# Optimization experiments

Hardware: AMD Instinct MI355X
Metric: run time of the kernel (lower is better)

## Reference

```python
import jax, jax.numpy as jnp
import numpy as np

H = 256  # LSTM hidden units per layer

def _cell(xt, h, c, W, U, b):
    # Keras LSTMCell: gate order i, f, g(cell), o; sigmoid recurrent activation, tanh activation
    z = xt @ W + h @ U + b  # (B, 4H)
    i, f, g, o = jnp.split(z, 4, axis=-1)
    c_new = jax.nn.sigmoid(f) * c + jax.nn.sigmoid(i) * jnp.tanh(g)
    h_new = jax.nn.sigmoid(o) * jnp.tanh(c_new)
    return h_new, c_new

def _stacked_lstm(x, W1, U1, b1, W2, U2, b2):
    # x: (B, T, F). Returns concat of FINAL CELL STATES of both layers: (B, 2H)
    # (original code takes outputs[i+1][1], i.e. the c state of each LSTMCell)
    B = x.shape[0]
    def step(carry, xt):
        h1, c1, h2, c2 = carry
        h1, c1 = _cell(xt, h1, c1, W1, U1, b1)
        h2, c2 = _cell(h1, h2, c2, W2, U2, b2)
        return (h1, c1, h2, c2), None
    z0 = jnp.zeros((B, H), x.dtype)
    (h1, c1, h2, c2), _ = jax.lax.scan(step, (z0, z0, z0, z0), jnp.swapaxes(x, 0, 1))
    return jnp.concatenate([c1, c2], axis=-1)

def _glorot(key, shape):
    lim = np.sqrt(6.0 / (shape[0] + shape[1]))
    return jax.random.uniform(key, shape, jnp.float32, -lim, lim)

def _lstm_bias():
    # Keras unit_forget_bias=True: forget-gate bias initialized to 1
    return jnp.zeros((4 * H,), jnp.float32).at[H:2 * H].set(1.0)

def setup_inputs():
    key = jax.random.key(0)
    ks = jax.random.split(key, 16)
    B, T, F, ZD = 16384, 20, 80, 32
    inp = {
        "x": jax.random.normal(ks[0], (B, T, F), jnp.float32),
        "eps1": jax.random.normal(ks[1], (B, ZD), jnp.float32),
        "eps2": jax.random.normal(ks[2], (B, ZD), jnp.float32),
        # z2 stacked LSTM (input F)
        "z2_W1": _glorot(ks[3], (F, 4 * H)), "z2_U1": _glorot(ks[4], (H, 4 * H)), "z2_b1": _lstm_bias(),
        "z2_W2": _glorot(ks[5], (H, 4 * H)), "z2_U2": _glorot(ks[6], (H, 4 * H)), "z2_b2": _lstm_bias(),
        # z1 stacked LSTM (input F + z2_dim)
        "z1_W1": _glorot(ks[7], (F + ZD, 4 * H)), "z1_U1": _glorot(ks[8], (H, 4 * H)), "z1_b1": _lstm_bias(),
        "z1_W2": _glorot(ks[9], (H, 4 * H)), "z1_U2": _glorot(ks[10], (H, 4 * H)), "z1_b2": _lstm_bias(),
        # dense heads (input 2H -> ZD), linear (mu_nl=logvar_nl=None)
        "mu2_W": _glorot(ks[11], (2 * H, ZD)), "mu2_b": jnp.zeros((ZD,), jnp.float32),
        "lv2_W": _glorot(ks[12], (2 * H, ZD)), "lv2_b": jnp.zeros((ZD,), jnp.float32),
        "mu1_W": _glorot(ks[13], (2 * H, ZD)), "mu1_b": jnp.zeros((ZD,), jnp.float32),
        "lv1_W": _glorot(ks[14], (2 * H, ZD)), "lv1_b": jnp.zeros((ZD,), jnp.float32),
    }
    return inp

def reference(x, eps1, eps2,
              z2_W1, z2_U1, z2_b1, z2_W2, z2_U2, z2_b2,
              z1_W1, z1_U1, z1_b1, z1_W2, z1_U2, z1_b2,
              mu2_W, mu2_b, lv2_W, lv2_b, mu1_W, mu1_b, lv1_W, lv1_b):
    B, T, _ = x.shape
    # z2 branch
    z2_pre = _stacked_lstm(x, z2_W1, z2_U1, z2_b1, z2_W2, z2_U2, z2_b2)  # (B, 2H)
    z2_mu = z2_pre @ mu2_W + mu2_b
    z2_logvar = z2_pre @ lv2_W + lv2_b
    z2_sample = eps2 * jnp.exp(0.5 * z2_logvar) + z2_mu  # reparameterize
    # z1 branch: tile z2_sample over time, concat with x
    z2_tiled = jnp.broadcast_to(z2_sample[:, None, :], (B, T, z2_sample.shape[-1]))
    x_z2 = jnp.concatenate([x, z2_tiled], axis=-1)  # (B, T, F+ZD)
    z1_pre = _stacked_lstm(x_z2, z1_W1, z1_U1, z1_b1, z1_W2, z1_U2, z1_b2)
    z1_mu = z1_pre @ mu1_W + mu1_b
    z1_logvar = z1_pre @ lv1_W + lv1_b
    z1_sample = eps1 * jnp.exp(0.5 * z1_logvar) + z1_mu
    return (z1_mu, z1_logvar, z1_sample, z2_mu, z2_logvar, z2_sample)
```

## Files before the change

kernel.cpp:

```cpp
#include <hip/hip_runtime.h>
#include <hip/hip_bf16.h>

#define B_SZ 16384
#define T_SZ 20

typedef __attribute__((ext_vector_type(8))) __bf16 bf16x8;
typedef __attribute__((ext_vector_type(4))) float f32x4;

__device__ __forceinline__ float sigm(float x){ return 1.f/(1.f+__expf(-x)); }
__device__ __forceinline__ float tanh_(float x){ return 1.f-2.f/(__expf(2.f*x)+1.f); }

#define OFF_L1Z2 0
#define OFF_L2Z2 360448
#define OFF_L1Z1 884736
#define OFF_L2Z1 1277952
#define OFF_HZ2  1802240
#define OFF_HZ1  1835008
#define WP_TOT   1867776

__global__ void prep_w(const float* __restrict__ W0, const float* __restrict__ U0,
                       const float* __restrict__ W1, const float* __restrict__ U1,
                       const float* __restrict__ W2, const float* __restrict__ U2,
                       const float* __restrict__ W3, const float* __restrict__ U3,
                       const float* __restrict__ muW2, const float* __restrict__ lvW2,
                       const float* __restrict__ muW1, const float* __restrict__ lvW1,
                       __bf16* __restrict__ wp)
{
    int idx = blockIdx.x * 256 + threadIdx.x;
    if (idx >= WP_TOT) return;
    if (idx < OFF_HZ2) {
        const float *W, *U;
        int Fx, Kx, KT, local;
        if (idx < OFF_L2Z2)      { W = W0; U = U0; Fx = 80;  Kx = 96;  KT = 11; local = idx; }
        else if (idx < OFF_L1Z1) { W = W1; U = U1; Fx = 256; Kx = 256; KT = 16; local = idx - OFF_L2Z2; }
        else if (idx < OFF_L2Z1) { W = W2; U = U2; Fx = 112; Kx = 128; KT = 12; local = idx - OFF_L1Z1; }
        else                     { W = W3; U = U3; Fx = 256; Kx = 256; KT = 16; local = idx - OFF_L2Z1; }
        int jj = local & 7, lane = (local >> 3) & 63, nt8 = (local >> 9) & 7, rest = local >> 12;
        int kt = rest % KT, wgn = rest / KT;
        int gate = nt8 >> 1, hh = nt8 & 1;
        int n = gate * 256 + wgn * 32 + hh * 16 + (lane & 15);
        int k = kt * 32 + ((lane >> 4) << 3) + jj;
        float v = (k < Fx) ? W[k * 1024 + n] : (k < Kx ? 0.f : U[(k - Kx) * 1024 + n]);
        wp[idx] = (__bf16)v;
    } else {
        int base = (idx < OFF_HZ1) ? OFF_HZ2 : OFF_HZ1;
        const float* mw = (idx < OFF_HZ1) ? muW2 : muW1;
        const float* lw = (idx < OFF_HZ1) ? lvW2 : lvW1;
        int local = idx - base;
        int jj = local & 7, lane = (local >> 3) & 63, nt = (local >> 9) & 3, kt = local >> 11;
        int k = kt * 32 + ((lane >> 4) << 3) + jj;
        int c16 = lane & 15;
        float v = (nt < 2) ? mw[k * 32 + nt * 16 + c16] : lw[k * 32 + (nt - 2) * 16 + c16];
        wp[idx] = (__bf16)v;
    }
}

__global__ void xconv(const float* __restrict__ x, __bf16* __restrict__ xb)
{
    int idx = blockIdx.x * 256 + threadIdx.x;
    int c8 = idx & 15, row = idx >> 4;
    bf16x8 r;
    if (c8 < 10) {
        const float4* p = reinterpret_cast<const float4*>(x + (size_t)row * 80 + c8 * 8);
        float4 u0 = p[0], u1 = p[1];
        r[0]=(__bf16)u0.x; r[1]=(__bf16)u0.y; r[2]=(__bf16)u0.z; r[3]=(__bf16)u0.w;
        r[4]=(__bf16)u1.x; r[5]=(__bf16)u1.y; r[6]=(__bf16)u1.z; r[7]=(__bf16)u1.w;
    } else {
#pragma unroll
        for (int i = 0; i < 8; ++i) r[i] = (__bf16)0.f;
    }
    *reinterpret_cast<bf16x8*>(xb + (size_t)row * 128 + c8 * 8) = r;
}

__global__ void bcast_z2(const __bf16* __restrict__ z2sb, __bf16* __restrict__ xb)
{
    int idx = blockIdx.x * 256 + threadIdx.x;
    int g = idx & 3, b = idx >> 2;
    bf16x8 v = *reinterpret_cast<const bf16x8*>(z2sb + (size_t)b * 32 + g * 8);
#pragma unroll
    for (int t = 0; t < T_SZ; ++t)
        *reinterpret_cast<bf16x8*>(xb + ((size_t)b * T_SZ + t) * 128 + 80 + g * 8) = v;
}

__device__ __forceinline__ void stage16(const __bf16* g, __bf16* l)
{
    __builtin_amdgcn_global_load_lds(
        (const __attribute__((address_space(1))) unsigned*)g,
        (__attribute__((address_space(3))) unsigned*)l, 16, 0, 0);
}

template <int KT, int KTP, int XKT, int TWOH, int FIRST>
__global__ void __launch_bounds__(256, 4)
step_gemm(const __bf16* __restrict__ xb, int t,
          const __bf16* __restrict__ hA, const __bf16* __restrict__ hB,
          const __bf16* __restrict__ wpm, const float* __restrict__ bias,
          float* __restrict__ cbuf, __bf16* __restrict__ hout)
{
    constexpr int P = (KT + 1) / 2;
    __shared__ __align__(16) __bf16 Bs[4][4096];

    const int tid = threadIdx.x;
    const int w = tid >> 6, lane = tid & 63;
    const int r16 = lane & 15, kq = lane >> 4;
    const int mid = blockIdx.x & 127, wgn = blockIdx.x >> 7;
    const int rb = mid * 128 + w * 32;
    const __bf16* wpB = wpm + (size_t)wgn * KTP * 4096;

    const __bf16 *x0 = nullptr, *x1 = nullptr;
    if (XKT > 0) {
        x0 = xb + ((size_t)(rb + r16) * T_SZ + t) * 128;
        x1 = xb + ((size_t)(rb + 16 + r16) * T_SZ + t) * 128;
    }
    const __bf16* hA0 = hA + (size_t)(rb + r16) * 256;
    const __bf16* hA1 = hA + (size_t)(rb + 16 + r16) * 256;
    const __bf16* hB0 = TWOH ? hB + (size_t)(rb + r16) * 256 : nullptr;
    const __bf16* hB1 = TWOH ? hB + (size_t)(rb + 16 + r16) * 256 : nullptr;

    f32x4 acc[8][2];
#pragma unroll
    for (int nt = 0; nt < 8; ++nt)
#pragma unroll
        for (int m = 0; m < 2; ++m) acc[nt][m] = f32x4{0.f, 0.f, 0.f, 0.f};

    auto aptr = [&](int kt, int m) -> const __bf16* {
        if (kt < XKT) return (m ? x1 : x0) + kt * 32 + kq * 8;
        int kk = kt - XKT;
        if (!TWOH || kk < 8) return (m ? hA1 : hA0) + kk * 32 + kq * 8;
        return (m ? hB1 : hB0) + (kk - 8) * 32 + kq * 8;
    };
    auto loadPh = [&](int k0, bf16x8* a) {
        a[0] = *reinterpret_cast<const bf16x8*>(aptr(k0, 0));
        a[1] = *reinterpret_cast<const bf16x8*>(aptr(k0, 1));
        if (k0 + 1 < KT) {
            a[2] = *reinterpret_cast<const bf16x8*>(aptr(k0 + 1, 0));
            a[3] = *reinterpret_cast<const bf16x8*>(aptr(k0 + 1, 1));
        }
    };
    auto compPh = [&](int k0, const bf16x8* a) {
        {
            const __bf16* bp = &Bs[k0 & 3][lane * 8];
#pragma unroll
            for (int nt = 0; nt < 8; ++nt) {
                bf16x8 bv = *reinterpret_cast<const bf16x8*>(bp + nt * 512);
                acc[nt][0] = __builtin_amdgcn_mfma_f32_16x16x32_bf16(a[0], bv, acc[nt][0], 0, 0, 0);
                acc[nt][1] = __builtin_amdgcn_mfma_f32_16x16x32_bf16(a[1], bv, acc[nt][1], 0, 0, 0);
            }
        }
        if (k0 + 1 < KT) {
            const __bf16* bp = &Bs[(k0 + 1) & 3][lane * 8];
#pragma unroll
            for (int nt = 0; nt < 8; ++nt) {
                bf16x8 bv = *reinterpret_cast<const bf16x8*>(bp + nt * 512);
                acc[nt][0] = __builtin_amdgcn_mfma_f32_16x16x32_bf16(a[2], bv, acc[nt][0], 0, 0, 0);
                acc[nt][1] = __builtin_amdgcn_mfma_f32_16x16x32_bf16(a[3], bv, acc[nt][1], 0, 0, 0);
            }
        }
    };
    auto stageKt = [&](int kt) {
        const __bf16* g = wpB + (size_t)kt * 4096 + tid * 8;
        stage16(g, &Bs[kt & 3][tid * 8]);
        stage16(g + 2048, &Bs[kt & 3][2048 + tid * 8]);
    };

    bf16x8 aP[2][4];
    stageKt(0);
    if (KT > 1) stageKt(1);
    loadPh(0, aP[0]);
    __syncthreads();

#pragma unroll
    for (int p = 0; p < P; ++p) {
        const int ks = 2 * p + 2;
        if (ks < KT)     stageKt(ks);
        if (ks + 1 < KT) stageKt(ks + 1);
        if (ks < KT)     loadPh(ks, aP[(p + 1) & 1]);
        compPh(2 * p, aP[p & 1]);
        __syncthreads();
    }

    float bg[2][4];
#pragma unroll
    for (int hh = 0; hh < 2; ++hh)
#pragma unroll
        for (int gate = 0; gate < 4; ++gate)
            bg[hh][gate] = bias[gate * 256 + wgn * 32 + hh * 16 + r16];

#pragma unroll
    for (int m = 0; m < 2; ++m)
#pragma unroll
        for (int hh = 0; hh < 2; ++hh) {
            const int hcol = wgn * 32 + hh * 16 + r16;
            f32x4 zi = acc[0 + hh][m], zf = acc[2 + hh][m], zg = acc[4 + hh][m], zo = acc[6 + hh][m];
#pragma unroll
            for (int q = 0; q < 4; ++q) {
                int row = rb + m * 16 + kq * 4 + q;
                size_t off = (size_t)row * 256 + hcol;
                float cn;
                if (FIRST) {
                    cn = sigm(zi[q] + bg[hh][0]) * tanh_(zg[q] + bg[hh][2]);
                } else {
                    float co = cbuf[off];
                    cn = sigm(zf[q] + bg[hh][1]) * co
                       + sigm(zi[q] + bg[hh][0]) * tanh_(zg[q] + bg[hh][2]);
                }
                cbuf[off] = cn;
                hout[off] = (__bf16)(sigm(zo[q] + bg[hh][3]) * tanh_(cn));
            }
        }
}

__global__ void __launch_bounds__(128, 4)
head_mfma(const float* __restrict__ c1, const float* __restrict__ c2,
          const __bf16* __restrict__ hp, const float* __restrict__ mub,
          const float* __restrict__ lvb, const float* __restrict__ eps,
          float* __restrict__ omu, float* __restrict__ olv, float* __restrict__ osm,
          __bf16* __restrict__ osb)
{
    const int tid = threadIdx.x;
    const int w = tid >> 6, lane = tid & 63;
    const int r16 = lane & 15, kq = lane >> 4;
    const int rb = blockIdx.x * 64 + w * 32;

    f32x4 acc[4][2];
#pragma unroll
    for (int nt = 0; nt < 4; ++nt)
#pragma unroll
        for (int m = 0; m < 2; ++m) acc[nt][m] = f32x4{0.f, 0.f, 0.f, 0.f};

#pragma unroll
    for (int kt = 0; kt < 16; ++kt) {
        const float* cs = (kt < 8) ? c1 : c2;
        int k = (kt & 7) * 32 + kq * 8;
        bf16x8 a[2];
#pragma unroll
        for (int m = 0; m < 2; ++m) {
            const float* pr = cs + (size_t)(rb + m * 16 + r16) * 256 + k;
            float4 u0 = reinterpret_cast<const float4*>(pr)[0];
            float4 u1 = reinterpret_cast<const float4*>(pr)[1];
            a[m][0]=(__bf16)u0.x; a[m][1]=(__bf16)u0.y; a[m][2]=(__bf16)u0.z; a[m][3]=(__bf16)u0.w;
            a[m][4]=(__bf16)u1.x; a[m][5]=(__bf16)u1.y; a[m][6]=(__bf16)u1.z; a[m][7]=(__bf16)u1.w;
        }
        const __bf16* hb = hp + kt * 2048 + lane * 8;
#pragma unroll
        for (int nt = 0; nt < 4; ++nt) {
            bf16x8 bv = *reinterpret_cast<const bf16x8*>(hb + nt * 512);
            acc[nt][0] = __builtin_amdgcn_mfma_f32_16x16x32_bf16(a[0], bv, acc[nt][0], 0, 0, 0);
            acc[nt][1] = __builtin_amdgcn_mfma_f32_16x16x32_bf16(a[1], bv, acc[nt][1], 0, 0, 0);
        }
    }

#pragma unroll
    for (int m = 0; m < 2; ++m)
#pragma unroll
        for (int q = 0; q < 4; ++q) {
            int row = rb + m * 16 + kq * 4 + q;
#pragma unroll
            for (int z = 0; z < 2; ++z) {
                int zc = z * 16 + r16;
                float mu = acc[z][m][q] + mub[zc];
                float lv = acc[z + 2][m][q] + lvb[zc];
                int idx = row * 32 + zc;
                omu[idx] = mu;
                olv[idx] = lv;
                float s = fmaf(eps[idx], expf(0.5f * lv), mu);
                osm[idx] = s;
                if (osb) osb[idx] = (__bf16)s;
            }
        }
}

extern "C" void kernel_launch(void* const* d_in, const int* in_sizes, int n_in,
                              void* d_out, int out_size, void* d_ws, size_t ws_size,
                              hipStream_t stream)
{
    const float* x    = (const float*)d_in[0];
    const float* eps1 = (const float*)d_in[1];
    const float* eps2 = (const float*)d_in[2];
    const float* z2W1 = (const float*)d_in[3];
    const float* z2U1 = (const float*)d_in[4];
    const float* z2b1 = (const float*)d_in[5];
    const float* z2W2 = (const float*)d_in[6];
    const float* z2U2 = (const float*)d_in[7];
    const float* z2b2 = (const float*)d_in[8];
    const float* z1W1 = (const float*)d_in[9];
    const float* z1U1 = (const float*)d_in[10];
    const float* z1b1 = (const float*)d_in[11];
    const float* z1W2 = (const float*)d_in[12];
    const float* z1U2 = (const float*)d_in[13];
    const float* z1b2 = (const float*)d_in[14];
    const float* mu2W = (const float*)d_in[15];
    const float* mu2b = (const float*)d_in[16];
    const float* lv2W = (const float*)d_in[17];
    const float* lv2b = (const float*)d_in[18];
    const float* mu1W = (const float*)d_in[19];
    const float* mu1b = (const float*)d_in[20];
    const float* lv1W = (const float*)d_in[21];
    const float* lv1b = (const float*)d_in[22];

    char* ws = (char*)d_ws;
    __bf16* wp   = (__bf16*)ws;
    __bf16* z2sb = (__bf16*)(ws + 4194304);
    __bf16* xb   = (__bf16*)(ws + 5242880);
    __bf16* h1a  = (__bf16*)(ws + 89128960);
    __bf16* h2a  = (__bf16*)(ws + 97517568);
    __bf16* h1b  = (__bf16*)(ws + 105906176);
    __bf16* h2b  = (__bf16*)(ws + 114294784);
    float*  c1   = (float*)(ws + 122683392);
    float*  c2   = (float*)(ws + 139460608);

    __bf16* h1[2] = {h1a, h1b};
    __bf16* h2[2] = {h2a, h2b};

    float* out = (float*)d_out;
    const int BZ = B_SZ * 32;
    float* z1mu = out;           float* z1lv = out + BZ;     float* z1sm = out + 2 * BZ;
    float* z2mu = out + 3 * BZ;  float* z2lv = out + 4 * BZ; float* z2sm = out + 5 * BZ;

    xconv<<<B_SZ * T_SZ * 16 / 256, 256, 0, stream>>>(x, xb);
    prep_w<<<7296, 256, 0, stream>>>(z2W1, z2U1, z2W2, z2U2, z1W1, z1U1, z1W2, z1U2,
                                     mu2W, lv2W, mu1W, lv1W, wp);

    step_gemm<3, 11, 3, 0, 1><<<1024, 256, 0, stream>>>(xb, 0, h1a, nullptr,
                                                        wp + OFF_L1Z2, z2b1, c1, h1[0]);
    step_gemm<8, 16, 0, 1, 1><<<1024, 256, 0, stream>>>(xb, 0, h1[0], h2a,
                                                        wp + OFF_L2Z2, z2b2, c2, h2[0]);
    for (int t = 1; t < T_SZ; ++t) {
        int cur = t & 1, prv = cur ^ 1;
        step_gemm<11, 11, 3, 0, 0><<<1024, 256, 0, stream>>>(xb, t, h1[prv], nullptr,
                                                             wp + OFF_L1Z2, z2b1, c1, h1[cur]);
        step_gemm<16, 16, 0, 1, 0><<<1024, 256, 0, stream>>>(xb, t, h1[cur], h2[prv],
                                                             wp + OFF_L2Z2, z2b2, c2, h2[cur]);
    }
    head_mfma<<<256, 128, 0, stream>>>(c1, c2, wp + OFF_HZ2, mu2b, lv2b, eps2,
                                       z2mu, z2lv, z2sm, z2sb);
    bcast_z2<<<B_SZ * 4 / 256, 256, 0, stream>>>(z2sb, xb);

    step_gemm<4, 12, 4, 0, 1><<<1024, 256, 0, stream>>>(xb, 0, h1a, nullptr,
                                                        wp + OFF_L1Z1, z1b1, c1, h1[0]);
    step_gemm<8, 16, 0, 1, 1><<<1024, 256, 0, stream>>>(xb, 0, h1[0], h2a,
                                                        wp + OFF_L2Z1, z1b2, c2, h2[0]);
    for (int t = 1; t < T_SZ; ++t) {
        int cur = t & 1, prv = cur ^ 1;
        step_gemm<12, 12, 4, 0, 0><<<1024, 256, 0, stream>>>(xb, t, h1[prv], nullptr,
                                                             wp + OFF_L1Z1, z1b1, c1, h1[cur]);
        step_gemm<16, 16, 0, 1, 0><<<1024, 256, 0, stream>>>(xb, t, h1[cur], h2[prv],
                                                             wp + OFF_L2Z1, z1b2, c2, h2[cur]);
    }
    head_mfma<<<256, 128, 0, stream>>>(c1, c2, wp + OFF_HZ1, mu1b, lv1b, eps1,
                                       z1mu, z1lv, z1sm, nullptr);
}
```

Before: 2.373 ms.

## Restructure step GEMM k-loop into per-tile pipeline with fine-grained vmcnt waits

Replaces the two-k-tile phase loop with a per-k-tile software pipeline that prefetches weights and A fragments two tiles ahead. It uses explicit s_waitcnt vmcnt counts plus a raw s_barrier and sched_barriers instead of __syncthreads, so outstanding loads for later tiles are not drained each step. It also folds the kq offset into the base pointers. The LDS ring has 4 slots with a distance-2 prefetch, which looks safe, but the hand-computed vmcnt values assume a fixed ordering of load instructions. If the compiler emits loads in a different order, correctness or overlap could suffer.

```diff
diff --git a/kernel.cpp b/kernel.cpp
--- a/kernel.cpp
+++ b/kernel.cpp
@@ -96,7 +96,6 @@
           const __bf16* __restrict__ wpm, const float* __restrict__ bias,
           float* __restrict__ cbuf, __bf16* __restrict__ hout)
 {
-    constexpr int P = (KT + 1) / 2;
     __shared__ __align__(16) __bf16 Bs[4][4096];
 
     const int tid = threadIdx.x;
@@ -108,13 +107,16 @@
 
     const __bf16 *x0 = nullptr, *x1 = nullptr;
     if (XKT > 0) {
-        x0 = xb + ((size_t)(rb + r16) * T_SZ + t) * 128;
-        x1 = xb + ((size_t)(rb + 16 + r16) * T_SZ + t) * 128;
-    }
-    const __bf16* hA0 = hA + (size_t)(rb + r16) * 256;
-    const __bf16* hA1 = hA + (size_t)(rb + 16 + r16) * 256;
-    const __bf16* hB0 = TWOH ? hB + (size_t)(rb + r16) * 256 : nullptr;
-    const __bf16* hB1 = TWOH ? hB + (size_t)(rb + 16 + r16) * 256 : nullptr;
+        x0 = xb + ((size_t)(rb + r16) * T_SZ + t) * 128 + kq * 8;
+        x1 = xb + ((size_t)(rb + 16 + r16) * T_SZ + t) * 128 + kq * 8;
+    }
+    const __bf16* hA0 = hA + (size_t)(rb + r16) * 256 + kq * 8;
+    const __bf16* hA1 = hA + (size_t)(rb + 16 + r16) * 256 + kq * 8;
+    const __bf16 *hB0 = nullptr, *hB1 = nullptr;
+    if (TWOH) {
+        hB0 = hB + (size_t)(rb + r16) * 256 + kq * 8;
+        hB1 = hB + (size_t)(rb + 16 + r16) * 256 + kq * 8;
+    }
 
     f32x4 acc[8][2];
 #pragma unroll
@@ -122,61 +124,44 @@
 #pragma unroll
         for (int m = 0; m < 2; ++m) acc[nt][m] = f32x4{0.f, 0.f, 0.f, 0.f};
 
-    auto aptr = [&](int kt, int m) -> const __bf16* {
-        if (kt < XKT) return (m ? x1 : x0) + kt * 32 + kq * 8;
+    bf16x8 aR[3][2];
+
+    auto ap = [&](int kt, int m) -> const __bf16* {
+        if (XKT > 0 && kt < XKT) return (m ? x1 : x0) + kt * 32;
         int kk = kt - XKT;
-        if (!TWOH || kk < 8) return (m ? hA1 : hA0) + kk * 32 + kq * 8;
-        return (m ? hB1 : hB0) + (kk - 8) * 32 + kq * 8;
+        if (!TWOH || kk < 8) return (m ? hA1 : hA0) + kk * 32;
+        return (m ? hB1 : hB0) + (kk - 8) * 32;
     };
-    auto loadPh = [&](int k0, bf16x8* a) {
-        a[0] = *reinterpret_cast<const bf16x8*>(aptr(k0, 0));
-        a[1] = *reinterpret_cast<const bf16x8*>(aptr(k0, 1));
-        if (k0 + 1 < KT) {
-            a[2] = *reinterpret_cast<const bf16x8*>(aptr(k0 + 1, 0));
-            a[3] = *reinterpret_cast<const bf16x8*>(aptr(k0 + 1, 1));
-        }
-    };
-    auto compPh = [&](int k0, const bf16x8* a) {
-        {
-            const __bf16* bp = &Bs[k0 & 3][lane * 8];
-#pragma unroll
-            for (int nt = 0; nt < 8; ++nt) {
-                bf16x8 bv = *reinterpret_cast<const bf16x8*>(bp + nt * 512);
-                acc[nt][0] = __builtin_amdgcn_mfma_f32_16x16x32_bf16(a[0], bv, acc[nt][0], 0, 0, 0);
-                acc[nt][1] = __builtin_amdgcn_mfma_f32_16x16x32_bf16(a[1], bv, acc[nt][1], 0, 0, 0);
-            }
-        }
-        if (k0 + 1 < KT) {
-            const __bf16* bp = &Bs[(k0 + 1) & 3][lane * 8];
-#pragma unroll
-            for (int nt = 0; nt < 8; ++nt) {
-                bf16x8 bv = *reinterpret_cast<const bf16x8*>(bp + nt * 512);
-                acc[nt][0] = __builtin_amdgcn_mfma_f32_16x16x32_bf16(a[2], bv, acc[nt][0], 0, 0, 0);
-                acc[nt][1] = __builtin_amdgcn_mfma_f32_16x16x32_bf16(a[3], bv, acc[nt][1], 0, 0, 0);
-            }
-        }
-    };
-    auto stageKt = [&](int kt) {
-        const __bf16* g = wpB + (size_t)kt * 4096 + tid * 8;
-        stage16(g, &Bs[kt & 3][tid * 8]);
-        stage16(g + 2048, &Bs[kt & 3][2048 + tid * 8]);
-    };
-
-    bf16x8 aP[2][4];
-    stageKt(0);
-    if (KT > 1) stageKt(1);
-    loadPh(0, aP[0]);
-    __syncthreads();
-
-#pragma unroll
-    for (int p = 0; p < P; ++p) {
-        const int ks = 2 * p + 2;
-        if (ks < KT)     stageKt(ks);
-        if (ks + 1 < KT) stageKt(ks + 1);
-        if (ks < KT)     loadPh(ks, aP[(p + 1) & 1]);
-        compPh(2 * p, aP[p & 1]);
-        __syncthreads();
-    }
+
+#define STG(K) { const __bf16* g_ = wpB + (size_t)(K) * 4096 + tid * 8;            \
+                 stage16(g_, &Bs[(K) & 3][tid * 8]);                               \
+                 stage16(g_ + 2048, &Bs[(K) & 3][2048 + tid * 8]); }
+#define LDA(K) { aR[(K) % 3][0] = *reinterpret_cast<const bf16x8*>(ap((K), 0));    \
+                 aR[(K) % 3][1] = *reinterpret_cast<const bf16x8*>(ap((K), 1)); }
+#define CMP(K) { const __bf16* bp_ = &Bs[(K) & 3][lane * 8];                       \
+    _Pragma("unroll") for (int nt = 0; nt < 8; ++nt) {                             \
+        bf16x8 bv_ = *reinterpret_cast<const bf16x8*>(bp_ + nt * 512);             \
+        acc[nt][0] = __builtin_amdgcn_mfma_f32_16x16x32_bf16(aR[(K)%3][0], bv_, acc[nt][0], 0, 0, 0); \
+        acc[nt][1] = __builtin_amdgcn_mfma_f32_16x16x32_bf16(aR[(K)%3][1], bv_, acc[nt][1], 0, 0, 0); } }
+#define PH(K) if constexpr ((K) < KT) {                                            \
+    __builtin_amdgcn_sched_barrier(0);                                             \
+    if constexpr ((K) + 2 < KT) { STG((K) + 2); LDA((K) + 2); }                    \
+    { constexpr int cnt_ = 4 * (((K) + 1 < KT) ? 1 : 0) + 4 * (((K) + 2 < KT) ? 1 : 0); \
+      asm volatile("s_waitcnt vmcnt(%0)" :: "n"(cnt_) : "memory"); }               \
+    __builtin_amdgcn_s_barrier();                                                  \
+    __builtin_amdgcn_sched_barrier(0);                                             \
+    CMP(K); }
+
+    STG(0); LDA(0);
+    if constexpr (KT > 1) { STG(1); LDA(1); }
+
+    PH(0)  PH(1)  PH(2)  PH(3)  PH(4)  PH(5)  PH(6)  PH(7)
+    PH(8)  PH(9)  PH(10) PH(11) PH(12) PH(13) PH(14) PH(15)
+
+#undef STG
+#undef LDA
+#undef CMP
+#undef PH
 
     float bg[2][4];
 #pragma unroll
```

After: 2.223 ms. 6.3% less time.
